# Optimization experiments

Measured on AMD Instinct MI355X. Metric: run time of the kernel, lower is better.

Reference implementation:

```python
import jax, jax.numpy as jnp
import numpy as np
import math

MEMORY_SIZE = 50000
FEATURE_SIZE = 4096  # = 64*8*8
HASH_SIZE = 128
B, C, H, W = 64, 64, 8, 8


def setup_inputs() -> dict:
    key = jax.random.key(0)
    k1, k2, k3, k4 = jax.random.split(key, 4)
    stdv = 1.0 / math.sqrt(FEATURE_SIZE)
    feature = jax.random.normal(k1, (B, C, H, W), dtype=jnp.float32)
    memory = jax.random.uniform(k2, (MEMORY_SIZE, FEATURE_SIZE), minval=-stdv, maxval=stdv, dtype=jnp.float32)
    # nn.Linear default init: U(-1/sqrt(fan_in), 1/sqrt(fan_in))
    hash_W = jax.random.uniform(k3, (HASH_SIZE, FEATURE_SIZE), minval=-stdv, maxval=stdv, dtype=jnp.float32)
    hash_b = jax.random.uniform(k4, (HASH_SIZE,), minval=-stdv, maxval=stdv, dtype=jnp.float32)
    return {"feature": feature, "memory": memory, "hash_W": hash_W, "hash_b": hash_b}


def _binarize(x, hash_W, hash_b):
    # 0.5 * (sign(Linear(x) - 0.5) + 1)  -> values in {0, 1} (0.5 only on measure-zero ties)
    return 0.5 * (jnp.sign(x @ hash_W.T + hash_b - 0.5) + 1.0)


def reference(feature, memory, hash_W, hash_b):
    b, c, h, w = feature.shape
    flat = feature.reshape(b, c * h * w)                      # [B, F]
    hm = _binarize(memory, hash_W, hash_b)                    # [M, 128]
    hf = _binarize(flat, hash_W, hash_b)                      # [B, 128]
    # For binary a,b: |a - b| = a + b - 2ab, so the L1 (Hamming) distance is a GEMM:
    HD = (hf.sum(-1, keepdims=True) + hm.sum(-1)[None, :]
          - 2.0 * (hf @ hm.T))                                # [B, M]
    idx = jnp.argmin(HD, axis=1)                              # [B]
    recon = memory[idx]                                       # gather nearest memory rows
    return recon.reshape(b, c, h, w)
```

## Files before the change

### kernel.cpp

```cpp
#include <hip/hip_runtime.h>
#include <hip/hip_bf16.h>
#include <stdint.h>
#include <stddef.h>

typedef __attribute__((ext_vector_type(8))) short s8v;
typedef __attribute__((ext_vector_type(4))) float f32x4;
typedef __attribute__((ext_vector_type(4))) uint32_t u32x4;

#define KDIM 4096
#define NH   128
#define MMEM 50000
#define BFEAT 64
#define NGRP 3125
#define NBLK 256
#define NGMAX 13
#define MLANES 512

static __device__ __forceinline__ short f2bfs(float f) {
  __hip_bfloat16 h = __float2bfloat16(f);
  short s;
  __builtin_memcpy(&s, &h, sizeof(s));
  return s;
}


__global__ __launch_bounds__(512, 2) void hash_bits_kernel(
    const float* __restrict__ A,
    const float* __restrict__ Wf,
    const float* __restrict__ hb,
    uint32_t* __restrict__ out_bits) {
  __shared__ short Abuf[2][NGMAX * 16 * 64];
  __shared__ unsigned short smb[NGMAX * 16][8];

  const int t    = threadIdx.x;
  const int lane = t & 63;
  const int w    = t >> 6;
  const int l15  = lane & 15;
  const int kq   = lane >> 4;
  const int b    = blockIdx.x;
  const int koff = b & 63;
  const int g0   = (b * NGRP) >> 8;
  const int NG   = (((b + 1) * NGRP) >> 8) - g0;
  const int row0 = g0 * 16;

  const float* srcA[4];
  int ldsoff[4];
#pragma unroll
  for (int p = 0; p < 4; ++p) {
    int P  = t + 512 * p;
    int g  = P >> 7;
    int q  = P & 127;
    int r  = q >> 3;
    int kg = q & 7;
    srcA[p]   = A + (size_t)(row0 + g * 16 + r) * KDIM + kg * 8;
    ldsoff[p] = (g * 16 + r) * 64 + ((kg ^ (r & 7)) << 3);
  }
  const bool v3 = (t + 1536) < NG * 128;

  const float* pbf = Wf + (size_t)(16 * w + l15) * KDIM + kq * 8;
  const float hbv = hb[16 * w + l15];

  f32x4 acc[NGMAX];
#pragma unroll
  for (int g = 0; g < NGMAX; ++g) acc[g] = (f32x4){0.f, 0.f, 0.f, 0.f};

  f32x4 aR[4][2];
  f32x4 bA[4], bB[4];

#define PCH(S) (((S) + koff) & 63)

#define LOADA(CH) do {                                                        \
  const f32x4* q0 = reinterpret_cast<const f32x4*>(srcA[0] + (CH) * 64);      \
  aR[0][0] = q0[0]; aR[0][1] = q0[1];                                         \
  const f32x4* q1 = reinterpret_cast<const f32x4*>(srcA[1] + (CH) * 64);      \
  aR[1][0] = q1[0]; aR[1][1] = q1[1];                                         \
  const f32x4* q2 = reinterpret_cast<const f32x4*>(srcA[2] + (CH) * 64);      \
  aR[2][0] = q2[0]; aR[2][1] = q2[1];                                         \
  if (v3) {                                                                   \
    const f32x4* q3 = reinterpret_cast<const f32x4*>(srcA[3] + (CH) * 64);    \
    aR[3][0] = q3[0]; aR[3][1] = q3[1];                                       \
  }                                                                           \
} while (0)

#define CVTW1(P, BUFW) do {                                                   \
  s8v av;                                                                     \
  av[0] = f2bfs(aR[P][0][0]); av[1] = f2bfs(aR[P][0][1]);                     \
  av[2] = f2bfs(aR[P][0][2]); av[3] = f2bfs(aR[P][0][3]);                     \
  av[4] = f2bfs(aR[P][1][0]); av[5] = f2bfs(aR[P][1][1]);                     \
  av[6] = f2bfs(aR[P][1][2]); av[7] = f2bfs(aR[P][1][3]);                     \
  *reinterpret_cast<s8v*>(&(BUFW)[ldsoff[P]]) = av;                           \
} while (0)

#define CVTWRITE(BUFW) do {                                                   \
  CVTW1(0, BUFW); CVTW1(1, BUFW); CVTW1(2, BUFW);                             \
  if (v3) CVTW1(3, BUFW);                                                     \
} while (0)

#define LOADB(CH, SET) do {                                                   \
  const f32x4* qb0 = reinterpret_cast<const f32x4*>(pbf + (CH) * 64);         \
  SET[0] = qb0[0]; SET[1] = qb0[1];                                           \
  const f32x4* qb1 = reinterpret_cast<const f32x4*>(pbf + (CH) * 64 + 32);    \
  SET[2] = qb1[0]; SET[3] = qb1[1];                                           \
} while (0)

#define COMPUTE(BUFR, SET) do {                                               \
  s8v b0, b1;                                                                 \
  b0[0] = f2bfs(SET[0][0]); b0[1] = f2bfs(SET[0][1]);                         \
  b0[2] = f2bfs(SET[0][2]); b0[3] = f2bfs(SET[0][3]);                         \
  b0[4] = f2bfs(SET[1][0]); b0[5] = f2bfs(SET[1][1]);                         \
  b0[6] = f2bfs(SET[1][2]); b0[7] = f2bfs(SET[1][3]);                         \
  b1[0] = f2bfs(SET[2][0]); b1[1] = f2bfs(SET[2][1]);                         \
  b1[2] = f2bfs(SET[2][2]); b1[3] = f2bfs(SET[2][3]);                         \
  b1[4] = f2bfs(SET[3][0]); b1[5] = f2bfs(SET[3][1]);                         \
  b1[6] = f2bfs(SET[3][2]); b1[7] = f2bfs(SET[3][3]);                         \
  _Pragma("unroll")                                                           \
  for (int g = 0; g < NGMAX; ++g) {                                           \
    const s8v af = *reinterpret_cast<const s8v*>(                             \
        &(BUFR)[(g * 16 + l15) * 64 + ((kq ^ (l15 & 7)) << 3)]);              \
    acc[g] = __builtin_amdgcn_mfma_f32_16x16x32_bf16(af, b0, acc[g], 0, 0, 0);\
  }                                                                           \
  _Pragma("unroll")                                                           \
  for (int g = 0; g < NGMAX; ++g) {                                           \
    const s8v af = *reinterpret_cast<const s8v*>(                             \
        &(BUFR)[(g * 16 + l15) * 64 + (((4 + kq) ^ (l15 & 7)) << 3)]);        \
    acc[g] = __builtin_amdgcn_mfma_f32_16x16x32_bf16(af, b1, acc[g], 0, 0, 0);\
  }                                                                           \
} while (0)

#define BARRIER() do {                                                        \
  asm volatile("s_waitcnt lgkmcnt(0)" ::: "memory");                          \
  __builtin_amdgcn_s_barrier();                                               \
  __builtin_amdgcn_sched_barrier(0);                                          \
} while (0)

#define STEP(S, BUFR, BUFW, SET) do {                                         \
  BARRIER();                                                                  \
  COMPUTE(BUFR, SET);                                                         \
  if ((S) + 1 < 64) CVTWRITE(BUFW);                                           \
  if ((S) + 2 < 64) { LOADA(PCH((S) + 2)); LOADB(PCH((S) + 2), SET); }        \
} while (0)

  LOADA(PCH(0));
  CVTWRITE(Abuf[0]);
  LOADA(PCH(1));
  LOADB(PCH(0), bA);
  LOADB(PCH(1), bB);

  for (int s2 = 0; s2 < 64; s2 += 2) {
    STEP(s2 + 0, Abuf[0], Abuf[1], bA);
    STEP(s2 + 1, Abuf[1], Abuf[0], bB);
  }

#pragma unroll
  for (int g = 0; g < NGMAX; ++g) {
#pragma unroll
    for (int r = 0; r < 4; ++r) {
      uint64_t mask = __ballot(acc[g][r] + hbv - 0.5f > 0.f);
      if (l15 == r)
        smb[g * 16 + (lane >> 4) * 4 + r][w] =
            (unsigned short)((mask >> (16 * (lane >> 4))) & 0xFFFFu);
    }
  }
  __syncthreads();
  const int rows = NG * 16;
  if (t < rows) {
    uint32_t w0 = (uint32_t)smb[t][0] | ((uint32_t)smb[t][1] << 16);
    uint32_t w1 = (uint32_t)smb[t][2] | ((uint32_t)smb[t][3] << 16);
    uint32_t w2 = (uint32_t)smb[t][4] | ((uint32_t)smb[t][5] << 16);
    uint32_t w3 = (uint32_t)smb[t][6] | ((uint32_t)smb[t][7] << 16);
    reinterpret_cast<u32x4*>(out_bits)[row0 + t] = (u32x4){w0, w1, w2, w3};
  }
}

__global__ __launch_bounds__(512) void argmin_gather_kernel(
    const uint32_t* __restrict__ hm_bits, const float* __restrict__ feature,
    const float* __restrict__ Wf, const float* __restrict__ hb,
    const float* __restrict__ memory, float* __restrict__ out) {
  __shared__ unsigned char hfb[NH];
  __shared__ uint32_t red[MLANES];
  const int b    = blockIdx.x;
  const int t    = threadIdx.x;
  const int w    = t >> 6;
  const int lane = t & 63;

  const f32x4* fv = reinterpret_cast<const f32x4*>(feature + (size_t)b * KDIM);
#pragma unroll 2
  for (int d = 0; d < 16; ++d) {
    const int n = w * 16 + d;
    const f32x4* wv = reinterpret_cast<const f32x4*>(Wf + (size_t)n * KDIM);
    float s = 0.f;
#pragma unroll 4
    for (int q = 0; q < 16; ++q) {
      f32x4 x = fv[lane + 64 * q], y = wv[lane + 64 * q];
      s += x[0] * y[0] + x[1] * y[1] + x[2] * y[2] + x[3] * y[3];
    }
    for (int o = 32; o; o >>= 1) s += __shfl_down(s, o, 64);
    if (lane == 0) hfb[n] = (s + hb[n] - 0.5f) > 0.f ? 1 : 0;
  }
  __syncthreads();

  uint64_t hf0 = 0, hf1 = 0;
  for (int c = 0; c < 64; ++c) {
    hf0 |= (uint64_t)(hfb[c] & 1u) << c;
    hf1 |= (uint64_t)(hfb[c + 64] & 1u) << c;
  }
  int hfsum = __popcll(hf0) + __popcll(hf1);
  uint32_t best = 0xFFFFFFFFu;
  for (int m = t; m < MMEM; m += MLANES) {
    u32x4 pv = reinterpret_cast<const u32x4*>(hm_bits)[m];
    uint64_t h0 = (uint64_t)pv[0] | ((uint64_t)pv[1] << 32);
    uint64_t h1 = (uint64_t)pv[2] | ((uint64_t)pv[3] << 32);
    int hmsum = __popcll(h0) + __popcll(h1);
    int dot   = __popcll(h0 & hf0) + __popcll(h1 & hf1);
    int hd    = hfsum + hmsum - 2 * dot;
    uint32_t key = ((uint32_t)hd << 16) | (uint32_t)m;
    best = best < key ? best : key;
  }
  red[t] = best;
  __syncthreads();
  for (int s = MLANES / 2; s > 0; s >>= 1) {
    if (t < s) red[t] = red[t] < red[t + s] ? red[t] : red[t + s];
    __syncthreads();
  }
  const int m = (int)(red[0] & 0xFFFFu);
  const f32x4* src = reinterpret_cast<const f32x4*>(memory + (size_t)m * KDIM);
  f32x4* dst = reinterpret_cast<f32x4*>(out + (size_t)b * KDIM);
  dst[t]       = src[t];
  dst[t + 512] = src[t + 512];
}

extern "C" void kernel_launch(void* const* d_in, const int* in_sizes, int n_in,
                              void* d_out, int out_size, void* d_ws, size_t ws_size,
                              hipStream_t stream) {
  const float* feature = (const float*)d_in[0];
  const float* memory  = (const float*)d_in[1];
  const float* hash_W  = (const float*)d_in[2];
  const float* hash_b  = (const float*)d_in[3];
  float* out = (float*)d_out;

  uint32_t* hm_bits = (uint32_t*)d_ws;

  hash_bits_kernel<<<NBLK, 512, 0, stream>>>(memory, hash_W, hash_b, hm_bits);
  argmin_gather_kernel<<<BFEAT, 512, 0, stream>>>(hm_bits, feature, hash_W,
                                                  hash_b, memory, out);
}
```

Before: 213.9 us.

## Screen memory rows by norm bound before computing exact hash bits

Replaces the bf16 MFMA hash GEMM over all memory rows with a Cauchy-Schwarz screen. Per-row squared norms are compared against the minimum of (0.5-b_j)^2/|w_j|^2, and rows that cannot set any bit get zero bits directly. Only the surviving rows go through an exact fp32 dot-product kernel, found via an atomic-appended list. The pass over memory becomes a pure streaming norm read instead of a GEMM. Cost then depends on how many rows survive the screen, which is data-dependent.

```diff
diff --git a/kernel.cpp b/kernel.cpp
--- a/kernel.cpp
+++ b/kernel.cpp
@@ -1,9 +1,7 @@
 #include <hip/hip_runtime.h>
-#include <hip/hip_bf16.h>
 #include <stdint.h>
 #include <stddef.h>
 
-typedef __attribute__((ext_vector_type(8))) short s8v;
 typedef __attribute__((ext_vector_type(4))) float f32x4;
 typedef __attribute__((ext_vector_type(4))) uint32_t u32x4;
 
@@ -11,164 +9,97 @@
 #define NH   128
 #define MMEM 50000
 #define BFEAT 64
-#define NGRP 3125
-#define NBLK 256
-#define NGMAX 13
 #define MLANES 512
 
-static __device__ __forceinline__ short f2bfs(float f) {
-  __hip_bfloat16 h = __float2bfloat16(f);
-  short s;
-  __builtin_memcpy(&s, &h, sizeof(s));
-  return s;
+__global__ __launch_bounds__(64) void wnorm_kernel(
+    const float* __restrict__ W, const float* __restrict__ hb,
+    float* __restrict__ ratsq, int* __restrict__ count) {
+  const int j    = blockIdx.x;
+  const int lane = threadIdx.x;
+  const f32x4* wv = reinterpret_cast<const f32x4*>(W + (size_t)j * KDIM);
+  float s = 0.f;
+#pragma unroll
+  for (int q = 0; q < 16; ++q) {
+    f32x4 v = wv[lane + 64 * q];
+    s += v[0] * v[0] + v[1] * v[1] + v[2] * v[2] + v[3] * v[3];
+  }
+  for (int o = 32; o; o >>= 1) s += __shfl_down(s, o, 64);
+  if (lane == 0) {
+    float margin = 0.5f - hb[j];
+    ratsq[j] = (margin > 0.f) ? (margin * margin / s) : -1.f;
+    if (j == 0) *count = 0;
+  }
 }
 
+__global__ __launch_bounds__(512) void rowscreen_kernel(
+    const float* __restrict__ A, const float* __restrict__ ratsq,
+    int* __restrict__ count, int* __restrict__ list,
+    u32x4* __restrict__ hm_bits) {
+  __shared__ float rs[NH];
+  const int t = threadIdx.x;
+  if (t < NH) rs[t] = ratsq[t];
+  __syncthreads();
+  float minrat = rs[0];
+  for (int j = 1; j < NH; ++j) minrat = fminf(minrat, rs[j]);
 
-__global__ __launch_bounds__(512, 2) void hash_bits_kernel(
-    const float* __restrict__ A,
-    const float* __restrict__ Wf,
-    const float* __restrict__ hb,
-    uint32_t* __restrict__ out_bits) {
-  __shared__ short Abuf[2][NGMAX * 16 * 64];
-  __shared__ unsigned short smb[NGMAX * 16][8];
-
-  const int t    = threadIdx.x;
+  const int gw   = blockIdx.x * 8 + (t >> 6);
   const int lane = t & 63;
-  const int w    = t >> 6;
-  const int l15  = lane & 15;
-  const int kq   = lane >> 4;
-  const int b    = blockIdx.x;
-  const int koff = b & 63;
-  const int g0   = (b * NGRP) >> 8;
-  const int NG   = (((b + 1) * NGRP) >> 8) - g0;
-  const int row0 = g0 * 16;
-
-  const float* srcA[4];
-  int ldsoff[4];
+  for (int row = gw; row < MMEM; row += 2048) {
+    const f32x4* rv = reinterpret_cast<const f32x4*>(A + (size_t)row * KDIM);
+    float s0 = 0.f, s1 = 0.f;
 #pragma unroll
-  for (int p = 0; p < 4; ++p) {
-    int P  = t + 512 * p;
-    int g  = P >> 7;
-    int q  = P & 127;
-    int r  = q >> 3;
-    int kg = q & 7;
-    srcA[p]   = A + (size_t)(row0 + g * 16 + r) * KDIM + kg * 8;
-    ldsoff[p] = (g * 16 + r) * 64 + ((kg ^ (r & 7)) << 3);
-  }
-  const bool v3 = (t + 1536) < NG * 128;
-
-  const float* pbf = Wf + (size_t)(16 * w + l15) * KDIM + kq * 8;
-  const float hbv = hb[16 * w + l15];
-
-  f32x4 acc[NGMAX];
-#pragma unroll
-  for (int g = 0; g < NGMAX; ++g) acc[g] = (f32x4){0.f, 0.f, 0.f, 0.f};
-
-  f32x4 aR[4][2];
-  f32x4 bA[4], bB[4];
-
-#define PCH(S) (((S) + koff) & 63)
-
-#define LOADA(CH) do {                                                        \
-  const f32x4* q0 = reinterpret_cast<const f32x4*>(srcA[0] + (CH) * 64);      \
-  aR[0][0] = q0[0]; aR[0][1] = q0[1];                                         \
-  const f32x4* q1 = reinterpret_cast<const f32x4*>(srcA[1] + (CH) * 64);      \
-  aR[1][0] = q1[0]; aR[1][1] = q1[1];                                         \
-  const f32x4* q2 = reinterpret_cast<const f32x4*>(srcA[2] + (CH) * 64);      \
-  aR[2][0] = q2[0]; aR[2][1] = q2[1];                                         \
-  if (v3) {                                                                   \
-    const f32x4* q3 = reinterpret_cast<const f32x4*>(srcA[3] + (CH) * 64);    \
-    aR[3][0] = q3[0]; aR[3][1] = q3[1];                                       \
-  }                                                                           \
-} while (0)
-
-#define CVTW1(P, BUFW) do {                                                   \
-  s8v av;                                                                     \
-  av[0] = f2bfs(aR[P][0][0]); av[1] = f2bfs(aR[P][0][1]);                     \
-  av[2] = f2bfs(aR[P][0][2]); av[3] = f2bfs(aR[P][0][3]);                     \
-  av[4] = f2bfs(aR[P][1][0]); av[5] = f2bfs(aR[P][1][1]);                     \
-  av[6] = f2bfs(aR[P][1][2]); av[7] = f2bfs(aR[P][1][3]);                     \
-  *reinterpret_cast<s8v*>(&(BUFW)[ldsoff[P]]) = av;                           \
-} while (0)
-
-#define CVTWRITE(BUFW) do {                                                   \
-  CVTW1(0, BUFW); CVTW1(1, BUFW); CVTW1(2, BUFW);                             \
-  if (v3) CVTW1(3, BUFW);                                                     \
-} while (0)
-
-#define LOADB(CH, SET) do {                                                   \
-  const f32x4* qb0 = reinterpret_cast<const f32x4*>(pbf + (CH) * 64);         \
-  SET[0] = qb0[0]; SET[1] = qb0[1];                                           \
-  const f32x4* qb1 = reinterpret_cast<const f32x4*>(pbf + (CH) * 64 + 32);    \
-  SET[2] = qb1[0]; SET[3] = qb1[1];                                           \
-} while (0)
-
-#define COMPUTE(BUFR, SET) do {                                               \
-  s8v b0, b1;                                                                 \
-  b0[0] = f2bfs(SET[0][0]); b0[1] = f2bfs(SET[0][1]);                         \
-  b0[2] = f2bfs(SET[0][2]); b0[3] = f2bfs(SET[0][3]);                         \
-  b0[4] = f2bfs(SET[1][0]); b0[5] = f2bfs(SET[1][1]);                         \
-  b0[6] = f2bfs(SET[1][2]); b0[7] = f2bfs(SET[1][3]);                         \
-  b1[0] = f2bfs(SET[2][0]); b1[1] = f2bfs(SET[2][1]);                         \
-  b1[2] = f2bfs(SET[2][2]); b1[3] = f2bfs(SET[2][3]);                         \
-  b1[4] = f2bfs(SET[3][0]); b1[5] = f2bfs(SET[3][1]);                         \
-  b1[6] = f2bfs(SET[3][2]); b1[7] = f2bfs(SET[3][3]);                         \
-  _Pragma("unroll")                                                           \
-  for (int g = 0; g < NGMAX; ++g) {                                           \
-    const s8v af = *reinterpret_cast<const s8v*>(                             \
-        &(BUFR)[(g * 16 + l15) * 64 + ((kq ^ (l15 & 7)) << 3)]);              \
-    acc[g] = __builtin_amdgcn_mfma_f32_16x16x32_bf16(af, b0, acc[g], 0, 0, 0);\
-  }                                                                           \
-  _Pragma("unroll")                                                           \
-  for (int g = 0; g < NGMAX; ++g) {                                           \
-    const s8v af = *reinterpret_cast<const s8v*>(                             \
-        &(BUFR)[(g * 16 + l15) * 64 + (((4 + kq) ^ (l15 & 7)) << 3)]);        \
-    acc[g] = __builtin_amdgcn_mfma_f32_16x16x32_bf16(af, b1, acc[g], 0, 0, 0);\
-  }                                                                           \
-} while (0)
-
-#define BARRIER() do {                                                        \
-  asm volatile("s_waitcnt lgkmcnt(0)" ::: "memory");                          \
-  __builtin_amdgcn_s_barrier();                                               \
-  __builtin_amdgcn_sched_barrier(0);                                          \
-} while (0)
-
-#define STEP(S, BUFR, BUFW, SET) do {                                         \
-  BARRIER();                                                                  \
-  COMPUTE(BUFR, SET);                                                         \
-  if ((S) + 1 < 64) CVTWRITE(BUFW);                                           \
-  if ((S) + 2 < 64) { LOADA(PCH((S) + 2)); LOADB(PCH((S) + 2), SET); }        \
-} while (0)
-
-  LOADA(PCH(0));
-  CVTWRITE(Abuf[0]);
-  LOADA(PCH(1));
-  LOADB(PCH(0), bA);
-  LOADB(PCH(1), bB);
-
-  for (int s2 = 0; s2 < 64; s2 += 2) {
-    STEP(s2 + 0, Abuf[0], Abuf[1], bA);
-    STEP(s2 + 1, Abuf[1], Abuf[0], bB);
-  }
-
-#pragma unroll
-  for (int g = 0; g < NGMAX; ++g) {
-#pragma unroll
-    for (int r = 0; r < 4; ++r) {
-      uint64_t mask = __ballot(acc[g][r] + hbv - 0.5f > 0.f);
-      if (l15 == r)
-        smb[g * 16 + (lane >> 4) * 4 + r][w] =
-            (unsigned short)((mask >> (16 * (lane >> 4))) & 0xFFFFu);
+    for (int q = 0; q < 16; q += 2) {
+      f32x4 v0 = rv[lane + 64 * q];
+      f32x4 v1 = rv[lane + 64 * (q + 1)];
+      s0 += v0[0] * v0[0] + v0[1] * v0[1] + v0[2] * v0[2] + v0[3] * v0[3];
+      s1 += v1[0] * v1[0] + v1[1] * v1[1] + v1[2] * v1[2] + v1[3] * v1[3];
+    }
+    float s = s0 + s1;
+    for (int o = 32; o; o >>= 1) s += __shfl_down(s, o, 64);
+    if (lane == 0) {
+      if (s * 1.0002f < minrat) {
+        hm_bits[row] = (u32x4){0u, 0u, 0u, 0u};
+      } else {
+        int i = atomicAdd(count, 1);
+        list[i] = row;
+      }
     }
   }
-  __syncthreads();
-  const int rows = NG * 16;
-  if (t < rows) {
-    uint32_t w0 = (uint32_t)smb[t][0] | ((uint32_t)smb[t][1] << 16);
-    uint32_t w1 = (uint32_t)smb[t][2] | ((uint32_t)smb[t][3] << 16);
-    uint32_t w2 = (uint32_t)smb[t][4] | ((uint32_t)smb[t][5] << 16);
-    uint32_t w3 = (uint32_t)smb[t][6] | ((uint32_t)smb[t][7] << 16);
-    reinterpret_cast<u32x4*>(out_bits)[row0 + t] = (u32x4){w0, w1, w2, w3};
+}
+
+__global__ __launch_bounds__(512) void exact_kernel(
+    const float* __restrict__ A, const float* __restrict__ W,
+    const float* __restrict__ hb, const int* __restrict__ count,
+    const int* __restrict__ list, uint32_t* __restrict__ hm_bits) {
+  __shared__ unsigned short sb[8];
+  const int w    = threadIdx.x >> 6;
+  const int lane = threadIdx.x & 63;
+  const int cnt  = *count;
+  for (int i = blockIdx.x; i < cnt; i += gridDim.x) {
+    const int row = list[i];
+    const f32x4* rv = reinterpret_cast<const f32x4*>(A + (size_t)row * KDIM);
+    unsigned short bits = 0;
+    for (int d = 0; d < 16; ++d) {
+      const int n = w * 16 + d;
+      const f32x4* wv = reinterpret_cast<const f32x4*>(W + (size_t)n * KDIM);
+      float s = 0.f;
+#pragma unroll 4
+      for (int q = 0; q < 16; ++q) {
+        f32x4 x = rv[lane + 64 * q], y = wv[lane + 64 * q];
+        s += x[0] * y[0] + x[1] * y[1] + x[2] * y[2] + x[3] * y[3];
+      }
+      for (int o = 32; o; o >>= 1) s += __shfl_down(s, o, 64);
+      s = __shfl(s, 0, 64);
+      if (s + hb[n] - 0.5f > 0.f) bits |= (unsigned short)(1u << d);
+    }
+    if (lane == 0) sb[w] = bits;
+    __syncthreads();
+    if (threadIdx.x < 4) {
+      uint32_t word = (uint32_t)sb[2 * threadIdx.x] |
+                      ((uint32_t)sb[2 * threadIdx.x + 1] << 16);
+      hm_bits[(size_t)row * 4 + threadIdx.x] = word;
+    }
+    __syncthreads();
   }
 }
 
@@ -238,9 +169,17 @@
   const float* hash_b  = (const float*)d_in[3];
   float* out = (float*)d_out;
 
-  uint32_t* hm_bits = (uint32_t*)d_ws;
+  char* ws = (char*)d_ws;
+  uint32_t* hm_bits = (uint32_t*)ws;
+  float*    ratsq   = (float*)(ws + 800000);
+  int*      count   = (int*)(ws + 800512);
+  int*      list    = (int*)(ws + 800768);
 
-  hash_bits_kernel<<<NBLK, 512, 0, stream>>>(memory, hash_W, hash_b, hm_bits);
+  wnorm_kernel<<<NH, 64, 0, stream>>>(hash_W, hash_b, ratsq, count);
+  rowscreen_kernel<<<256, 512, 0, stream>>>(memory, ratsq, count, list,
+                                            (u32x4*)hm_bits);
+  exact_kernel<<<128, 512, 0, stream>>>(memory, hash_W, hash_b, count, list,
+                                        hm_bits);
   argmin_gather_kernel<<<BFEAT, 512, 0, stream>>>(hm_bits, feature, hash_W,
                                                   hash_b, memory, out);
 }
```

Result: slower. 234.7 us (+9.7%).
